# Optimization experiments

Hardware: AMD Instinct MI355X
Metric: run time of the kernel (lower is better)

Reference implementation:

```python
import jax, jax.numpy as jnp
import numpy as np
import math

D, A, TOPK, EXPAND = 1024, 64, 32, 4
B, S = 2, 4096
DI = D * EXPAND


def setup_inputs() -> dict:
    key = jax.random.key(0)
    ks = jax.random.split(key, 32)
    w = lambda k, shape, fan_in: jax.random.normal(k, shape, jnp.float32) * (1.0 / np.sqrt(fan_in))
    u = lambda k: jax.random.uniform(k, (1, 1, D), jnp.float32)
    return {
        "x": jax.random.normal(ks[0], (B, S, D), jnp.float32),
        "norm1_w": jnp.ones((D,), jnp.float32),
        "tm_mix_k": u(ks[1]),
        "tm_mix_v": u(ks[2]),
        "tm_mix_r": u(ks[3]),
        "tm_key_w": w(ks[4], (D, D), D),
        "tm_value_w": w(ks[5], (D, D), D),
        "tm_recept_w": w(ks[6], (D, D), D),
        "tm_out_w": w(ks[7], (D, D), D),
        "sa_q_w": w(ks[8], (A, D), D),
        "sa_q_b": jnp.zeros((A,), jnp.float32),
        "sa_k_w": w(ks[9], (A, D), D),
        "sa_k_b": jnp.zeros((A,), jnp.float32),
        "sa_v_w": w(ks[10], (D, D), D),
        "sa_v_b": jnp.zeros((D,), jnp.float32),
        "sa_o_w": w(ks[11], (D, D), D),
        "sa_o_b": jnp.zeros((D,), jnp.float32),
        "norm2_w": jnp.ones((D,), jnp.float32),
        "cm_mix_k": u(ks[12]),
        "cm_mix_r": u(ks[13]),
        "cm_key_w": w(ks[14], (DI, D), D),
        "cm_recept_w": w(ks[15], (D, D), D),
        "cm_value_w": w(ks[16], (D, DI), DI),
    }


def _rmsnorm(x, w, eps=1e-8):
    norm = jnp.linalg.norm(x, axis=-1, keepdims=True) / np.sqrt(x.shape[-1])
    return w * x / (norm + eps)


def _token_shift(x):
    # torch.cat([x[:, 0:1], x[:, :-1]], dim=1)
    return jnp.concatenate([x[:, :1], x[:, :-1]], axis=1)


def _sparse_attn(x, qw, qb, kw, kb, vw, vb, ow, ob, topk):
    b, s, _ = x.shape
    a = qw.shape[0]
    Q = x @ qw.T + qb                                    # (b, s, a)
    K = x @ kw.T + kb                                    # (b, s, a)
    V = x @ vw.T + vb                                    # (b, s, d)
    scores = jnp.einsum('bqa,bka->bqk', Q, K) / math.sqrt(a)  # (b, s, s)
    if topk < s:
        vals, idx = jax.lax.top_k(scores, topk)          # (b, s, topk)
        sparse = jnp.full_like(scores, -jnp.inf)
        bi = jnp.arange(b)[:, None, None]
        si = jnp.arange(s)[None, :, None]
        sparse = sparse.at[bi, si, idx].set(vals)
        attn = jax.nn.softmax(sparse, axis=-1)
    else:
        attn = jax.nn.softmax(scores, axis=-1)
    out = jnp.einsum('bqk,bkd->bqd', attn, V)
    return out @ ow.T + ob


def _time_mix(x, mk, mv, mr, kw, vw, rw, ow, qw, qb, skw, skb, svw, svb, sow, sob, topk):
    xx = _token_shift(x)
    k = (x * mk + xx * (1 - mk)) @ kw.T
    v = (x * mv + xx * (1 - mv)) @ vw.T
    r = (x * mr + xx * (1 - mr)) @ rw.T
    attn_out = _sparse_attn(x, qw, qb, skw, skb, svw, svb, sow, sob, topk)
    rkv = jax.nn.sigmoid(r) * (attn_out + v)
    return rkv @ ow.T


def _channel_mix(x, mk, mr, kw, rw, vw):
    xx = _token_shift(x)
    k = (x * mk + xx * (1 - mk)) @ kw.T
    r = (x * mr + xx * (1 - mr)) @ rw.T
    k = jnp.square(jax.nn.relu(k))
    kv = k @ vw.T
    return jax.nn.sigmoid(r) * kv


def reference(x, norm1_w, tm_mix_k, tm_mix_v, tm_mix_r, tm_key_w, tm_value_w,
              tm_recept_w, tm_out_w, sa_q_w, sa_q_b, sa_k_w, sa_k_b, sa_v_w,
              sa_v_b, sa_o_w, sa_o_b, norm2_w, cm_mix_k, cm_mix_r, cm_key_w,
              cm_recept_w, cm_value_w):
    x = x + _time_mix(_rmsnorm(x, norm1_w), tm_mix_k, tm_mix_v, tm_mix_r,
                      tm_key_w, tm_value_w, tm_recept_w, tm_out_w,
                      sa_q_w, sa_q_b, sa_k_w, sa_k_b, sa_v_w, sa_v_b,
                      sa_o_w, sa_o_b, TOPK)
    x = x + _channel_mix(_rmsnorm(x, norm2_w), cm_mix_k, cm_mix_r,
                         cm_key_w, cm_recept_w, cm_value_w)
    return x
```

## Files before the change

### kernel.cpp

```cpp
#include <hip/hip_runtime.h>
#include <math.h>

typedef unsigned short u16;
using short8  = __attribute__((ext_vector_type(8))) short;
using float4v = __attribute__((ext_vector_type(4))) float;

__device__ __forceinline__ float b2f(u16 u) {
    union { unsigned int i; float f; } v; v.i = ((unsigned int)u) << 16; return v.f;
}
__device__ __forceinline__ u16 f2b(float f) {
    union { float f; unsigned int i; } v; v.f = f;
    unsigned int x = v.i;
    unsigned int r = (x + 0x7fffu + ((x >> 16) & 1u)) >> 16;
    return (u16)r;
}

#define GLOAD_LDS16(gp, lp) \
    __builtin_amdgcn_global_load_lds( \
        (const __attribute__((address_space(1))) unsigned int*)(gp), \
        (__attribute__((address_space(3))) unsigned int*)(lp), 16, 0, 0)

__global__ __launch_bounds__(256) void wcvt(const float* __restrict__ s,
                                            u16* __restrict__ d, int n) {
    int stride = gridDim.x * 256;
    for (int i = blockIdx.x * 256 + threadIdx.x; i < n; i += stride)
        d[i] = f2b(s[i]);
}

__global__ __launch_bounds__(256) void prep_qwT4(const float* __restrict__ qw,
                                                 float* __restrict__ qwT4) {
    int idx = blockIdx.x * 256 + threadIdx.x;
    int a = idx >> 10, d = idx & 1023;
    qwT4[(size_t)(d >> 2) * 256 + a * 4 + (d & 3)] = qw[idx];
}

__global__ __launch_bounds__(256) void mix2out(const float* __restrict__ src,
                                               const float* __restrict__ w,
                                               const float* __restrict__ f1,
                                               const float* __restrict__ f2,
                                               u16* __restrict__ out1,
                                               u16* __restrict__ out2) {
    __shared__ float redc[256], redp[256];
    int tid = threadIdx.x;
    size_t i = blockIdx.x;
    size_t ip = ((i & 4095) == 0) ? i : i - 1;
    float xc[4], xp[4];
    float ssc = 0.f, ssp = 0.f;
#pragma unroll
    for (int l = 0; l < 4; ++l) {
        int d = tid + l * 256;
        xc[l] = src[i * 1024 + d];  ssc += xc[l] * xc[l];
        xp[l] = src[ip * 1024 + d]; ssp += xp[l] * xp[l];
    }
    redc[tid] = ssc; redp[tid] = ssp; __syncthreads();
    for (int st = 128; st > 0; st >>= 1) {
        if (tid < st) { redc[tid] += redc[tid + st]; redp[tid] += redp[tid + st]; }
        __syncthreads();
    }
    float ic  = 1.f / (sqrtf(redc[0]) * (1.f / 32.f) + 1e-8f);
    float ipv = 1.f / (sqrtf(redp[0]) * (1.f / 32.f) + 1e-8f);
#pragma unroll
    for (int l = 0; l < 4; ++l) {
        int d = tid + l * 256;
        float wd = w[d];
        float xn = wd * xc[l] * ic;
        float xx = wd * xp[l] * ipv;
        float fa = f1[d], fb = f2[d];
        out1[i * 1024 + d] = f2b(fa * xn + (1.f - fa) * xx);
        out2[i * 1024 + d] = f2b(fb * xn + (1.f - fb) * xx);
    }
}

__global__ __launch_bounds__(256) void kproj(const float* __restrict__ x,
                                             const float* __restrict__ w1,
                                             const float* __restrict__ kw,
                                             const float* __restrict__ kb,
                                             float* __restrict__ Kt4,
                                             float* __restrict__ invn) {
    __shared__ double xk[1024];
    __shared__ double red[256];
    int tid = threadIdx.x;
    size_t j = blockIdx.x;
    double ss = 0.0;
    float xc[4];
#pragma unroll
    for (int l = 0; l < 4; ++l) {
        int d = tid + l * 256;
        xc[l] = x[j * 1024 + d];
        ss += (double)xc[l] * (double)xc[l];
    }
    red[tid] = ss; __syncthreads();
    for (int st = 128; st > 0; st >>= 1) {
        if (tid < st) red[tid] += red[tid + st];
        __syncthreads();
    }
    double inv = 1.0 / (sqrt(red[0]) * (1.0 / 32.0) + 1e-8);
#pragma unroll
    for (int l = 0; l < 4; ++l) {
        int d = tid + l * 256;
        xk[d] = (double)w1[d] * (double)xc[l] * inv;
    }
    __syncthreads();
    int wv = tid >> 6, lane = tid & 63;
    int b = (int)(j >> 12), jj = (int)(j & 4095);
    for (int it = 0; it < 16; ++it) {
        int a = wv * 16 + it;
        const float* kr = kw + (size_t)a * 1024;
        double p = 0.0;
#pragma unroll
        for (int m = 0; m < 16; ++m) p += xk[lane + 64 * m] * (double)kr[lane + 64 * m];
        for (int off = 32; off; off >>= 1) p += __shfl_xor(p, off);
        if (lane == 0)
            Kt4[(((size_t)b * 16 + (a >> 2)) * 4096 + jj) * 4 + (a & 3)] = (float)(p + (double)kb[a]);
    }
    if (tid == 0) invn[j] = (float)inv;
}

__global__ __attribute__((amdgpu_waves_per_eu(2, 4)))
__launch_bounds__(64) void attn_w(const float* __restrict__ x,
                                  const float* __restrict__ w1,
                                  const float* __restrict__ qwT4,
                                  const float* __restrict__ qb,
                                  const float* __restrict__ Kt4,
                                  const float* __restrict__ invn,
                                  u16* __restrict__ y) {
    __shared__ _Float16 sc[4096];
    __shared__ double qv64s[64];
    __shared__ int    candL[40];
    __shared__ float  pwL[32];
    __shared__ int    idxL[32];

    int lane = threadIdx.x;
    int i = blockIdx.x;
    int b = i >> 12;
    int base = b << 12;

    const float* xr = x + (size_t)i * 1024;
    double qp0 = 0.0, qp1 = 0.0, qp2 = 0.0, qp3 = 0.0;
#pragma unroll 4
    for (int d4 = 0; d4 < 256; ++d4) {
        float4 w4  = *(const float4*)(w1 + d4 * 4);
        float4 x4  = *(const float4*)(xr + d4 * 4);
        float4 qw4 = *(const float4*)(qwT4 + (size_t)d4 * 256 + lane * 4);
        qp0 += (double)(w4.x * x4.x) * (double)qw4.x;
        qp1 += (double)(w4.y * x4.y) * (double)qw4.y;
        qp2 += (double)(w4.z * x4.z) * (double)qw4.z;
        qp3 += (double)(w4.w * x4.w) * (double)qw4.w;
    }
    double q = ((qp0 + qp1) + (qp2 + qp3)) * (double)invn[i] + (double)qb[lane];
    qv64s[lane] = q;
    float qf = (float)q;

    float4 qreg[16];
#pragma unroll
    for (int g = 0; g < 16; ++g) {
        qreg[g].x = __shfl(qf, 4 * g + 0);
        qreg[g].y = __shfl(qf, 4 * g + 1);
        qreg[g].z = __shfl(qf, 4 * g + 2);
        qreg[g].w = __shfl(qf, 4 * g + 3);
    }

    const float4* K4 = (const float4*)Kt4 + (size_t)b * 16 * 4096;
    float4 kva[16], kvb[16];
    float lv1 = -3.4e38f, lv2 = -3.4e38f;
    int   li1 = 0x7ffffffe, li2 = 0x7fffffff;
#pragma unroll
    for (int g = 0; g < 16; ++g) kva[g] = K4[g * 4096 + lane];

#define SCORE_PROC(BUF, JEXPR)                                                  \
    {                                                                           \
        int j_ = (JEXPR);                                                       \
        float s_ = 0.f;                                                         \
        _Pragma("unroll")                                                       \
        for (int g = 0; g < 16; ++g)                                            \
            s_ += qreg[g].x * BUF[g].x + qreg[g].y * BUF[g].y                   \
                + qreg[g].z * BUF[g].z + qreg[g].w * BUF[g].w;                  \
        s_ *= 0.125f;                                                           \
        if (!(s_ == s_)) s_ = -65000.0f;                                        \
        _Float16 h_ = (_Float16)s_;                                             \
        s_ = (float)h_;                                                         \
        sc[j_] = h_;                                                            \
        if (s_ > lv1 || (s_ == lv1 && j_ < li1)) {                              \
            lv2 = lv1; li2 = li1; lv1 = s_; li1 = j_;                           \
        } else if (s_ > lv2 || (s_ == lv2 && j_ < li2)) { lv2 = s_; li2 = j_; } \
    }

#pragma unroll 1
    for (int t = 0; t < 64; t += 2) {
        int j1 = (t + 1) * 64 + lane;
#pragma unroll
        for (int g = 0; g < 16; ++g) kvb[g] = K4[g * 4096 + j1];
        __builtin_amdgcn_sched_barrier(0);
        SCORE_PROC(kva, t * 64 + lane);
        __builtin_amdgcn_sched_barrier(0);
        if (t + 2 < 64) {
            int j2 = (t + 2) * 64 + lane;
#pragma unroll
            for (int g = 0; g < 16; ++g) kva[g] = K4[g * 4096 + j2];
        }
        __builtin_amdgcn_sched_barrier(0);
        SCORE_PROC(kvb, j1);
        __builtin_amdgcn_sched_barrier(0);
    }
#undef SCORE_PROC

    bool v2ok = true;
    for (int it = 0; it < 40; ++it) {
        float mv = lv1; int mi = li1;
#pragma unroll
        for (int off = 32; off >= 1; off >>= 1) {
            float ov = __shfl_xor(mv, off); int oi = __shfl_xor(mi, off);
            if (ov > mv || (ov == mv && oi < mi)) { mv = ov; mi = oi; }
        }
        if (lane == 0) candL[it] = mi;
        if (li1 == mi) {
            sc[mi] = (_Float16)(-65504.0f);
            if (v2ok) { lv1 = lv2; li1 = li2; v2ok = false; }
            else {
                lv1 = -3.4e38f; li1 = 0x7ffffffe; lv2 = -3.4e38f; li2 = 0x7fffffff;
                for (int t = 0; t < 64; ++t) {
                    int j = t * 64 + lane;
                    float v = (float)sc[j];
                    if (v > lv1 || (v == lv1 && j < li1)) { lv2 = lv1; li2 = li1; lv1 = v; li1 = j; }
                    else if (v > lv2 || (v == lv2 && j < li2)) { lv2 = v; li2 = j; }
                }
                v2ok = true;
            }
        }
    }

    int c = (lane < 40) ? lane : 0;
    int j = candL[c];
    double s = 0.0;
#pragma unroll
    for (int g = 0; g < 16; ++g) {
        float4 kv = K4[g * 4096 + j];
        s += qv64s[4 * g + 0] * (double)kv.x + qv64s[4 * g + 1] * (double)kv.y
           + qv64s[4 * g + 2] * (double)kv.z + qv64s[4 * g + 3] * (double)kv.w;
    }
    s *= 0.125;
    if (lane >= 40) { s = -1.0e300; j = 0x7fffffff; }

    int rank = 0;
    for (int c2 = 0; c2 < 40; ++c2) {
        double s2 = __shfl(s, c2); int j2 = __shfl(j, c2);
        if (s2 > s || (s2 == s && j2 < j)) ++rank;
    }

    unsigned long long m0 = __ballot(rank == 0);
    int src = __ffsll((unsigned long long)m0) - 1;
    double mx = __shfl(s, src);
    double e = (rank < 32) ? exp(s - mx) : 0.0;
    double sum = e;
#pragma unroll
    for (int off = 1; off < 64; off <<= 1) sum += __shfl_xor(sum, off);
    if (rank < 32) {
        pwL[rank] = (float)(e / sum) * invn[base + j];
        idxL[rank] = j;
    }

    float acc[16], xga[16], xgb[16];
#pragma unroll
    for (int m = 0; m < 16; ++m) acc[m] = 0.f;
    {
        const float* x0 = x + (size_t)(base + idxL[0]) * 1024;
#pragma unroll
        for (int m = 0; m < 16; ++m) xga[m] = x0[m * 64 + lane];
    }
#pragma unroll 1
    for (int k = 0; k < 32; k += 2) {
        const float* xn1 = x + (size_t)(base + idxL[k + 1]) * 1024;
#pragma unroll
        for (int m = 0; m < 16; ++m) xgb[m] = xn1[m * 64 + lane];
        __builtin_amdgcn_sched_barrier(0);
        float p0 = pwL[k];
#pragma unroll
        for (int m = 0; m < 16; ++m) acc[m] += p0 * xga[m];
        __builtin_amdgcn_sched_barrier(0);
        if (k + 2 < 32) {
            const float* xn2 = x + (size_t)(base + idxL[k + 2]) * 1024;
#pragma unroll
            for (int m = 0; m < 16; ++m) xga[m] = xn2[m * 64 + lane];
        }
        __builtin_amdgcn_sched_barrier(0);
        float p1 = pwL[k + 1];
#pragma unroll
        for (int m = 0; m < 16; ++m) acc[m] += p1 * xgb[m];
        __builtin_amdgcn_sched_barrier(0);
    }
#pragma unroll
    for (int m = 0; m < 16; ++m) {
        int d = m * 64 + lane;
        y[(size_t)i * 1024 + d] = f2b(w1[d] * acc[m]);
    }
}

template <int EPI>
__global__ __launch_bounds__(256) void gemm_bt(const u16* __restrict__ A,
                                               const u16* __restrict__ B,
                                               u16* outB, float* outF,
                                               const float* __restrict__ biasF,
                                               const u16* aux0,
                                               const float* auxF,
                                               int N, int K, int lda, int ldb) {
    __shared__ u16 As[128 * 64];
    __shared__ u16 Bs[128 * 64];
    int tid = threadIdx.x;
    int lane = tid & 63;
    int wv = tid >> 6;

    int gx = gridDim.x, gy = gridDim.y;
    int nwg = gx * gy;
    int bx = blockIdx.x, by = blockIdx.y;
    if ((nwg & 7) == 0) {
        int hw = by * gx + bx;
        int q = nwg >> 3;
        int lg = (hw & 7) * q + (hw >> 3);
        bx = lg % gx;
        by = lg / gx;
    }

    int row0 = by * 128;
    int col0 = bx * 128;
    int wm = (wv >> 1) * 64;
    int wn = (wv & 1) * 64;
    int frow = lane & 15, quad = lane >> 4;

    float4v zero = {0.f, 0.f, 0.f, 0.f};
    float4v acc[4][4];
#pragma unroll
    for (int i = 0; i < 4; ++i)
#pragma unroll
        for (int j = 0; j < 4; ++j) acc[i][j] = zero;

    for (int k0 = 0; k0 < K; k0 += 64) {
#pragma unroll
        for (int it = 0; it < 4; ++it) {
            int base = (wv * 4 + it) * 512;
            int e = base + lane * 8;
            int r = e >> 6, c = e & 63;
            GLOAD_LDS16(A + (size_t)(row0 + r) * lda + (k0 + c), &As[base]);
            GLOAD_LDS16(B + (size_t)(col0 + r) * ldb + (k0 + c), &Bs[base]);
        }
        __syncthreads();
#pragma unroll
        for (int kk = 0; kk < 64; kk += 32) {
            short8 a_frag[4], b_frag[4];
#pragma unroll
            for (int mi = 0; mi < 4; ++mi)
                a_frag[mi] = *(const short8*)&As[(wm + mi * 16 + frow) * 64 + kk + quad * 8];
#pragma unroll
            for (int ni = 0; ni < 4; ++ni)
                b_frag[ni] = *(const short8*)&Bs[(wn + ni * 16 + frow) * 64 + kk + quad * 8];
#pragma unroll
            for (int mi = 0; mi < 4; ++mi)
#pragma unroll
                for (int ni = 0; ni < 4; ++ni)
                    acc[mi][ni] = __builtin_amdgcn_mfma_f32_16x16x32_bf16(
                        a_frag[mi], b_frag[ni], acc[mi][ni], 0, 0, 0);
        }
        __syncthreads();
    }

#pragma unroll
    for (int mi = 0; mi < 4; ++mi) {
#pragma unroll
        for (int ni = 0; ni < 4; ++ni) {
#pragma unroll
            for (int r = 0; r < 4; ++r) {
                int row = row0 + wm + mi * 16 + quad * 4 + r;
                int col = col0 + wn + ni * 16 + frow;
                size_t g = (size_t)row * N + col;
                float v = acc[mi][ni][r];
                if constexpr (EPI == 0) {
                    outB[g] = f2b(v + biasF[col]);
                } else if constexpr (EPI == 1) {
                    outB[g] = f2b(v + b2f(aux0[g]));
                } else if constexpr (EPI == 2) {
                    float sg = 1.f / (1.f + expf(-v));
                    outB[g] = f2b(sg * b2f(aux0[g]));
                } else if constexpr (EPI == 3) {
                    outF[g] = v + auxF[g];
                } else if constexpr (EPI == 4) {
                    outB[g] = f2b(1.f / (1.f + expf(-v)));
                } else if constexpr (EPI == 5) {
                    float t = v > 0.f ? v : 0.f;
                    outB[g] = f2b(t * t);
                } else if constexpr (EPI == 6) {
                    outF[g] = outF[g] + b2f(aux0[g]) * v;
                }
            }
        }
    }
}

extern "C" void kernel_launch(void* const* d_in, const int* in_sizes, int n_in,
                              void* d_out, int out_size, void* d_ws, size_t ws_size,
                              hipStream_t stream) {
    (void)in_sizes; (void)n_in; (void)out_size; (void)ws_size;
    const float* x   = (const float*)d_in[0];
    const float* n1w = (const float*)d_in[1];
    const float* tmv = (const float*)d_in[3];
    const float* tmr = (const float*)d_in[4];
    const float* vw  = (const float*)d_in[6];
    const float* rw  = (const float*)d_in[7];
    const float* ow  = (const float*)d_in[8];
    const float* qw  = (const float*)d_in[9];
    const float* qb  = (const float*)d_in[10];
    const float* skw = (const float*)d_in[11];
    const float* skb = (const float*)d_in[12];
    const float* svw = (const float*)d_in[13];
    const float* svb = (const float*)d_in[14];
    const float* sow = (const float*)d_in[15];
    const float* sob = (const float*)d_in[16];
    const float* n2w = (const float*)d_in[17];
    const float* cmk = (const float*)d_in[18];
    const float* cmr = (const float*)d_in[19];
    const float* ckw = (const float*)d_in[20];
    const float* crw = (const float*)d_in[21];
    const float* cvw = (const float*)d_in[22];

    char* W = (char*)d_ws;
    const size_t MB = 1ull << 20;
    u16*   bufA  = (u16*)(W + 0 * MB);
    u16*   bufB  = (u16*)(W + 16 * MB);
    u16*   bufC  = (u16*)(W + 32 * MB);
    u16*   bufD  = (u16*)(W + 48 * MB);
    float* Kt4   = (float*)(W + 64 * MB);
    float* invn  = (float*)(W + 66 * MB);
    float* qwT4  = (float*)(W + 67 * MB);
    u16*   ckw16 = (u16*)(W + 68 * MB);
    u16*   cvw16 = (u16*)(W + 76 * MB);
    u16*   svw16 = (u16*)(W + 84 * MB);
    u16*   sow16 = (u16*)(W + 86 * MB);
    u16*   vw16  = (u16*)(W + 88 * MB);
    u16*   rw16  = (u16*)(W + 90 * MB);
    u16*   ow16  = (u16*)(W + 92 * MB);
    u16*   crw16 = (u16*)(W + 94 * MB);
    float* x1    = (float*)d_out;

    dim3 blk(256);
    dim3 gN1024(8, 64);
    dim3 gN2048(16, 64);
    const int NW = 512;

    wcvt<<<NW, blk, 0, stream>>>(svw, svw16, 1024 * 1024);
    wcvt<<<NW, blk, 0, stream>>>(sow, sow16, 1024 * 1024);
    wcvt<<<NW, blk, 0, stream>>>(vw,  vw16,  1024 * 1024);
    wcvt<<<NW, blk, 0, stream>>>(rw,  rw16,  1024 * 1024);
    wcvt<<<NW, blk, 0, stream>>>(ow,  ow16,  1024 * 1024);
    wcvt<<<NW, blk, 0, stream>>>(crw, crw16, 1024 * 1024);
    wcvt<<<NW, blk, 0, stream>>>(ckw, ckw16, 4096 * 1024);
    wcvt<<<NW, blk, 0, stream>>>(cvw, cvw16, 1024 * 4096);
    prep_qwT4<<<256, blk, 0, stream>>>(qw, qwT4);

    mix2out<<<8192, blk, 0, stream>>>(x, n1w, tmv, tmr, bufA, bufC);
    kproj<<<8192, blk, 0, stream>>>(x, n1w, skw, skb, Kt4, invn);
    attn_w<<<8192, dim3(64), 0, stream>>>(x, n1w, qwT4, qb, Kt4, invn, bufB);
    gemm_bt<0><<<gN1024, blk, 0, stream>>>(bufB, svw16, bufD, nullptr, svb, nullptr, nullptr, 1024, 1024, 1024, 1024);
    gemm_bt<0><<<gN1024, blk, 0, stream>>>(bufD, sow16, bufB, nullptr, sob, nullptr, nullptr, 1024, 1024, 1024, 1024);
    gemm_bt<1><<<gN1024, blk, 0, stream>>>(bufA, vw16, bufB, nullptr, nullptr, bufB, nullptr, 1024, 1024, 1024, 1024);
    gemm_bt<2><<<gN1024, blk, 0, stream>>>(bufC, rw16, bufB, nullptr, nullptr, bufB, nullptr, 1024, 1024, 1024, 1024);
    gemm_bt<3><<<gN1024, blk, 0, stream>>>(bufB, ow16, nullptr, x1, nullptr, nullptr, x, 1024, 1024, 1024, 1024);

    mix2out<<<8192, blk, 0, stream>>>(x1, n2w, cmk, cmr, bufA, bufC);
    gemm_bt<4><<<gN1024, blk, 0, stream>>>(bufC, crw16, bufD, nullptr, nullptr, nullptr, nullptr, 1024, 1024, 1024, 1024);
    for (int c = 0; c < 2; ++c) {
        const u16* ckw_c = ckw16 + (size_t)c * 2048 * 1024;
        const u16* cvw_c = cvw16 + (size_t)c * 2048;
        gemm_bt<5><<<gN2048, blk, 0, stream>>>(bufA, ckw_c, bufB, nullptr, nullptr, nullptr, nullptr,
                                               2048, 1024, 1024, 1024);
        gemm_bt<6><<<gN1024, blk, 0, stream>>>(bufB, cvw_c, nullptr, x1, nullptr, bufD, nullptr,
                                               1024, 2048, 2048, 4096);
    }
}
```

Before: 1.553 ms.

## Compute attention scores with split-bf16 MFMA GEMM instead of per-row scalar dot products

Moves the Q projection into the K-projection kernel, which also emits hi/lo bf16 splits of Q and K. A new score_gemm kernel runs 3-term split-bf16 MFMA to build the full fp16 score matrix per batch, staged in the output buffer. The attention selection kernel then only reads the precomputed scores for its top-k scan. This removes the FP32 per-row score loop and the redundant Q computation from attention. In exchange it adds a 32MB-per-batch score round-trip through memory and a slight precision change in the scores, which could alter the selected top-k candidates.

```diff
diff --git a/kernel.cpp b/kernel.cpp
--- a/kernel.cpp
+++ b/kernel.cpp
@@ -25,13 +25,6 @@
     int stride = gridDim.x * 256;
     for (int i = blockIdx.x * 256 + threadIdx.x; i < n; i += stride)
         d[i] = f2b(s[i]);
-}
-
-__global__ __launch_bounds__(256) void prep_qwT4(const float* __restrict__ qw,
-                                                 float* __restrict__ qwT4) {
-    int idx = blockIdx.x * 256 + threadIdx.x;
-    int a = idx >> 10, d = idx & 1023;
-    qwT4[(size_t)(d >> 2) * 256 + a * 4 + (d & 3)] = qw[idx];
 }
 
 __global__ __launch_bounds__(256) void mix2out(const float* __restrict__ src,
@@ -75,8 +68,15 @@
                                              const float* __restrict__ w1,
                                              const float* __restrict__ kw,
                                              const float* __restrict__ kb,
+                                             const float* __restrict__ qw,
+                                             const float* __restrict__ qb,
                                              float* __restrict__ Kt4,
-                                             float* __restrict__ invn) {
+                                             float* __restrict__ invn,
+                                             double* __restrict__ qv64,
+                                             u16* __restrict__ Qhi,
+                                             u16* __restrict__ Qlo,
+                                             u16* __restrict__ Khi,
+                                             u16* __restrict__ Klo) {
     __shared__ double xk[1024];
     __shared__ double red[256];
     int tid = threadIdx.x;
@@ -110,20 +110,110 @@
 #pragma unroll
         for (int m = 0; m < 16; ++m) p += xk[lane + 64 * m] * (double)kr[lane + 64 * m];
         for (int off = 32; off; off >>= 1) p += __shfl_xor(p, off);
-        if (lane == 0)
-            Kt4[(((size_t)b * 16 + (a >> 2)) * 4096 + jj) * 4 + (a & 3)] = (float)(p + (double)kb[a]);
+        if (lane == 0) {
+            double kv = p + (double)kb[a];
+            Kt4[(((size_t)b * 16 + (a >> 2)) * 4096 + jj) * 4 + (a & 3)] = (float)kv;
+            float kf = (float)kv;
+            u16 hi = f2b(kf);
+            Khi[j * 64 + a] = hi;
+            Klo[j * 64 + a] = f2b(kf - b2f(hi));
+        }
+    }
+    for (int it = 0; it < 16; ++it) {
+        int a = wv * 16 + it;
+        const float* qr = qw + (size_t)a * 1024;
+        double p = 0.0;
+#pragma unroll
+        for (int m = 0; m < 16; ++m) p += xk[lane + 64 * m] * (double)qr[lane + 64 * m];
+        for (int off = 32; off; off >>= 1) p += __shfl_xor(p, off);
+        if (lane == 0) {
+            double qv = p + (double)qb[a];
+            qv64[j * 64 + a] = qv;
+            float qf = (float)qv;
+            u16 hi = f2b(qf);
+            Qhi[j * 64 + a] = hi;
+            Qlo[j * 64 + a] = f2b(qf - b2f(hi));
+        }
     }
     if (tid == 0) invn[j] = (float)inv;
 }
 
-__global__ __attribute__((amdgpu_waves_per_eu(2, 4)))
-__launch_bounds__(64) void attn_w(const float* __restrict__ x,
-                                  const float* __restrict__ w1,
-                                  const float* __restrict__ qwT4,
-                                  const float* __restrict__ qb,
-                                  const float* __restrict__ Kt4,
-                                  const float* __restrict__ invn,
-                                  u16* __restrict__ y) {
+__global__ __launch_bounds__(256) void score_gemm(const u16* __restrict__ Qh,
+                                                  const u16* __restrict__ Ql,
+                                                  const u16* __restrict__ Kh,
+                                                  const u16* __restrict__ Kl,
+                                                  _Float16* __restrict__ scp) {
+    __shared__ u16 Ah[128 * 64], Al[128 * 64], Bh[128 * 64], Bl[128 * 64];
+    int tid = threadIdx.x;
+    int lane = tid & 63;
+    int wv = tid >> 6;
+    int row0 = blockIdx.y * 128;
+    int col0 = blockIdx.x * 128;
+    int frow = lane & 15, quad = lane >> 4;
+
+#pragma unroll
+    for (int it = 0; it < 4; ++it) {
+        int base = (wv * 4 + it) * 512;
+        int e = base + lane * 8;
+        int r = e >> 6, c = e & 63;
+        GLOAD_LDS16(Qh + (size_t)(row0 + r) * 64 + c, &Ah[base]);
+        GLOAD_LDS16(Ql + (size_t)(row0 + r) * 64 + c, &Al[base]);
+        GLOAD_LDS16(Kh + (size_t)(col0 + r) * 64 + c, &Bh[base]);
+        GLOAD_LDS16(Kl + (size_t)(col0 + r) * 64 + c, &Bl[base]);
+    }
+    __syncthreads();
+
+    int wm = (wv >> 1) * 64;
+    int wn = (wv & 1) * 64;
+    float4v zero = {0.f, 0.f, 0.f, 0.f};
+    float4v acc[4][4];
+#pragma unroll
+    for (int i = 0; i < 4; ++i)
+#pragma unroll
+        for (int j = 0; j < 4; ++j) acc[i][j] = zero;
+
+#pragma unroll
+    for (int kk = 0; kk < 64; kk += 32) {
+        short8 ah[4], al[4], bh[4], bl[4];
+#pragma unroll
+        for (int mi = 0; mi < 4; ++mi) {
+            ah[mi] = *(const short8*)&Ah[(wm + mi * 16 + frow) * 64 + kk + quad * 8];
+            al[mi] = *(const short8*)&Al[(wm + mi * 16 + frow) * 64 + kk + quad * 8];
+        }
+#pragma unroll
+        for (int ni = 0; ni < 4; ++ni) {
+            bh[ni] = *(const short8*)&Bh[(wn + ni * 16 + frow) * 64 + kk + quad * 8];
+            bl[ni] = *(const short8*)&Bl[(wn + ni * 16 + frow) * 64 + kk + quad * 8];
+        }
+#pragma unroll
+        for (int mi = 0; mi < 4; ++mi)
+#pragma unroll
+            for (int ni = 0; ni < 4; ++ni) {
+                acc[mi][ni] = __builtin_amdgcn_mfma_f32_16x16x32_bf16(ah[mi], bh[ni], acc[mi][ni], 0, 0, 0);
+                acc[mi][ni] = __builtin_amdgcn_mfma_f32_16x16x32_bf16(ah[mi], bl[ni], acc[mi][ni], 0, 0, 0);
+                acc[mi][ni] = __builtin_amdgcn_mfma_f32_16x16x32_bf16(al[mi], bh[ni], acc[mi][ni], 0, 0, 0);
+            }
+    }
+
+#pragma unroll
+    for (int mi = 0; mi < 4; ++mi)
+#pragma unroll
+        for (int ni = 0; ni < 4; ++ni)
+#pragma unroll
+            for (int r = 0; r < 4; ++r) {
+                int row = row0 + wm + mi * 16 + quad * 4 + r;
+                int col = col0 + wn + ni * 16 + frow;
+                scp[(size_t)row * 4096 + col] = (_Float16)(0.125f * acc[mi][ni][r]);
+            }
+}
+
+__global__ __launch_bounds__(64) void attn_sel(const float* __restrict__ x,
+                                               const float* __restrict__ w1,
+                                               const _Float16* __restrict__ scp,
+                                               const double* __restrict__ qv64,
+                                               const float* __restrict__ Kt4,
+                                               const float* __restrict__ invn,
+                                               u16* __restrict__ y, int bb) {
     __shared__ _Float16 sc[4096];
     __shared__ double qv64s[64];
     __shared__ int    candL[40];
@@ -131,78 +221,29 @@
     __shared__ int    idxL[32];
 
     int lane = threadIdx.x;
-    int i = blockIdx.x;
+    int r = blockIdx.x;
+    int i = bb + r;
     int b = i >> 12;
     int base = b << 12;
 
-    const float* xr = x + (size_t)i * 1024;
-    double qp0 = 0.0, qp1 = 0.0, qp2 = 0.0, qp3 = 0.0;
-#pragma unroll 4
-    for (int d4 = 0; d4 < 256; ++d4) {
-        float4 w4  = *(const float4*)(w1 + d4 * 4);
-        float4 x4  = *(const float4*)(xr + d4 * 4);
-        float4 qw4 = *(const float4*)(qwT4 + (size_t)d4 * 256 + lane * 4);
-        qp0 += (double)(w4.x * x4.x) * (double)qw4.x;
-        qp1 += (double)(w4.y * x4.y) * (double)qw4.y;
-        qp2 += (double)(w4.z * x4.z) * (double)qw4.z;
-        qp3 += (double)(w4.w * x4.w) * (double)qw4.w;
-    }
-    double q = ((qp0 + qp1) + (qp2 + qp3)) * (double)invn[i] + (double)qb[lane];
-    qv64s[lane] = q;
-    float qf = (float)q;
-
-    float4 qreg[16];
-#pragma unroll
-    for (int g = 0; g < 16; ++g) {
-        qreg[g].x = __shfl(qf, 4 * g + 0);
-        qreg[g].y = __shfl(qf, 4 * g + 1);
-        qreg[g].z = __shfl(qf, 4 * g + 2);
-        qreg[g].w = __shfl(qf, 4 * g + 3);
-    }
-
-    const float4* K4 = (const float4*)Kt4 + (size_t)b * 16 * 4096;
-    float4 kva[16], kvb[16];
+    qv64s[lane] = qv64[(size_t)i * 64 + lane];
+
+    const short8* srow = (const short8*)(scp + (size_t)r * 4096);
+#pragma unroll
+    for (int t = 0; t < 8; ++t) {
+        short8 v = srow[t * 64 + lane];
+        *(short8*)&sc[(t * 64 + lane) * 8] = v;
+    }
+
     float lv1 = -3.4e38f, lv2 = -3.4e38f;
     int   li1 = 0x7ffffffe, li2 = 0x7fffffff;
-#pragma unroll
-    for (int g = 0; g < 16; ++g) kva[g] = K4[g * 4096 + lane];
-
-#define SCORE_PROC(BUF, JEXPR)                                                  \
-    {                                                                           \
-        int j_ = (JEXPR);                                                       \
-        float s_ = 0.f;                                                         \
-        _Pragma("unroll")                                                       \
-        for (int g = 0; g < 16; ++g)                                            \
-            s_ += qreg[g].x * BUF[g].x + qreg[g].y * BUF[g].y                   \
-                + qreg[g].z * BUF[g].z + qreg[g].w * BUF[g].w;                  \
-        s_ *= 0.125f;                                                           \
-        if (!(s_ == s_)) s_ = -65000.0f;                                        \
-        _Float16 h_ = (_Float16)s_;                                             \
-        s_ = (float)h_;                                                         \
-        sc[j_] = h_;                                                            \
-        if (s_ > lv1 || (s_ == lv1 && j_ < li1)) {                              \
-            lv2 = lv1; li2 = li1; lv1 = s_; li1 = j_;                           \
-        } else if (s_ > lv2 || (s_ == lv2 && j_ < li2)) { lv2 = s_; li2 = j_; } \
-    }
-
 #pragma unroll 1
-    for (int t = 0; t < 64; t += 2) {
-        int j1 = (t + 1) * 64 + lane;
-#pragma unroll
-        for (int g = 0; g < 16; ++g) kvb[g] = K4[g * 4096 + j1];
-        __builtin_amdgcn_sched_barrier(0);
-        SCORE_PROC(kva, t * 64 + lane);
-        __builtin_amdgcn_sched_barrier(0);
-        if (t + 2 < 64) {
-            int j2 = (t + 2) * 64 + lane;
-#pragma unroll
-            for (int g = 0; g < 16; ++g) kva[g] = K4[g * 4096 + j2];
-        }
-        __builtin_amdgcn_sched_barrier(0);
-        SCORE_PROC(kvb, j1);
-        __builtin_amdgcn_sched_barrier(0);
-    }
-#undef SCORE_PROC
+    for (int t = 0; t < 64; ++t) {
+        int j = t * 64 + lane;
+        float v = (float)sc[j];
+        if (v > lv1 || (v == lv1 && j < li1)) { lv2 = lv1; li2 = li1; lv1 = v; li1 = j; }
+        else if (v > lv2 || (v == lv2 && j < li2)) { lv2 = v; li2 = j; }
+    }
 
     bool v2ok = true;
     for (int it = 0; it < 40; ++it) {
@@ -229,6 +270,7 @@
         }
     }
 
+    const float4* K4 = (const float4*)Kt4 + (size_t)b * 16 * 4096;
     int c = (lane < 40) ? lane : 0;
     int j = candL[c];
     double s = 0.0;
@@ -426,9 +468,13 @@
     u16*   bufB  = (u16*)(W + 16 * MB);
     u16*   bufC  = (u16*)(W + 32 * MB);
     u16*   bufD  = (u16*)(W + 48 * MB);
+    double* qv64 = (double*)(W + 48 * MB);
+    u16*   Qhi   = (u16*)(W + 52 * MB);
+    u16*   Qlo   = (u16*)(W + 53 * MB);
+    u16*   Khi   = (u16*)(W + 54 * MB);
+    u16*   Klo   = (u16*)(W + 55 * MB);
     float* Kt4   = (float*)(W + 64 * MB);
     float* invn  = (float*)(W + 66 * MB);
-    float* qwT4  = (float*)(W + 67 * MB);
     u16*   ckw16 = (u16*)(W + 68 * MB);
     u16*   cvw16 = (u16*)(W + 76 * MB);
     u16*   svw16 = (u16*)(W + 84 * MB);
@@ -438,6 +484,7 @@
     u16*   ow16  = (u16*)(W + 92 * MB);
     u16*   crw16 = (u16*)(W + 94 * MB);
     float* x1    = (float*)d_out;
+    _Float16* scF = (_Float16*)d_out;
 
     dim3 blk(256);
     dim3 gN1024(8, 64);
@@ -452,11 +499,17 @@
     wcvt<<<NW, blk, 0, stream>>>(crw, crw16, 1024 * 1024);
     wcvt<<<NW, blk, 0, stream>>>(ckw, ckw16, 4096 * 1024);
     wcvt<<<NW, blk, 0, stream>>>(cvw, cvw16, 1024 * 4096);
-    prep_qwT4<<<256, blk, 0, stream>>>(qw, qwT4);
 
     mix2out<<<8192, blk, 0, stream>>>(x, n1w, tmv, tmr, bufA, bufC);
-    kproj<<<8192, blk, 0, stream>>>(x, n1w, skw, skb, Kt4, invn);
-    attn_w<<<8192, dim3(64), 0, stream>>>(x, n1w, qwT4, qb, Kt4, invn, bufB);
+    kproj<<<8192, blk, 0, stream>>>(x, n1w, skw, skb, qw, qb, Kt4, invn,
+                                    qv64, Qhi, Qlo, Khi, Klo);
+    for (int bb = 0; bb < 2; ++bb) {
+        size_t o = (size_t)bb * 4096 * 64;
+        score_gemm<<<dim3(32, 32), blk, 0, stream>>>(Qhi + o, Qlo + o,
+                                                     Khi + o, Klo + o, scF);
+        attn_sel<<<4096, dim3(64), 0, stream>>>(x, n1w, scF, qv64, Kt4, invn,
+                                                bufB, bb * 4096);
+    }
     gemm_bt<0><<<gN1024, blk, 0, stream>>>(bufB, svw16, bufD, nullptr, svb, nullptr, nullptr, 1024, 1024, 1024, 1024);
     gemm_bt<0><<<gN1024, blk, 0, stream>>>(bufD, sow16, bufB, nullptr, sob, nullptr, nullptr, 1024, 1024, 1024, 1024);
     gemm_bt<1><<<gN1024, blk, 0, stream>>>(bufA, vw16, bufB, nullptr, nullptr, bufB, nullptr, 1024, 1024, 1024, 1024);
```

Measured after the change: 1.301 ms. 1.19x faster.
